# Kernel optimization log

Measured on AMD Instinct MI355X. Metric: run time of the kernel, lower is better.

Reference implementation:

```python
import jax, jax.numpy as jnp
import numpy as np

# Poincare ball manifold with curvature c = 1.0 (as in HGCN / HADA)
C = 1.0
SQC = 1.0  # sqrt(c)
MIN_NORM = 1e-15
PROJ_EPS = 4e-3  # float32 boundary eps used by HGCN PoincareBall.proj


def _norm(x):
    return jnp.clip(jnp.linalg.norm(x, axis=-1, keepdims=True), MIN_NORM)


def artanh(x):
    return jnp.arctanh(jnp.clip(x, -1.0 + 1e-7, 1.0 - 1e-7))


def proj(x):
    n = _norm(x)
    maxnorm = (1.0 - PROJ_EPS) / SQC
    return jnp.where(n > maxnorm, x / n * maxnorm, x)


def proj_tan0(u):
    return u  # identity on the Poincare ball


def expmap0(u):
    n = _norm(u)
    return jnp.tanh(SQC * n) * u / (SQC * n)


def logmap0(p):
    n = _norm(p)
    return artanh(SQC * n) * p / (SQC * n)


def mobius_add(x, y):
    x2 = jnp.sum(x * x, axis=-1, keepdims=True)
    y2 = jnp.sum(y * y, axis=-1, keepdims=True)
    xy = jnp.sum(x * y, axis=-1, keepdims=True)
    num = (1.0 + 2.0 * C * xy + C * y2) * x + (1.0 - C * x2) * y
    den = 1.0 + 2.0 * C * xy + C * C * x2 * y2
    return num / jnp.clip(den, MIN_NORM)


def mobius_matvec(M, x):
    xn = _norm(x)
    mx = x @ M.T
    mxn = _norm(mx)
    res = jnp.tanh(mxn / xn * artanh(SQC * xn)) * mx / (mxn * SQC)
    is_zero = jnp.all(mx == 0.0, axis=-1, keepdims=True)
    return jnp.where(is_zero, jnp.zeros_like(res), res)


def lambda_x(x):
    return 2.0 / jnp.clip(1.0 - C * jnp.sum(x * x, axis=-1, keepdims=True), MIN_NORM)


def expmap(x, u):
    n = _norm(u)
    second = jnp.tanh(SQC * lambda_x(x) * n / 2.0) * u / (SQC * n)
    return mobius_add(x, second)


def logmap(x, y):
    sub = mobius_add(-x, y)
    n = _norm(sub)
    return 2.0 / (SQC * lambda_x(x)) * artanh(SQC * n) * sub / n


def setup_inputs() -> dict:
    key = jax.random.key(0)
    k1, k2, k3, k4, k5 = jax.random.split(key, 5)
    n, d_in, d_out = 1024, 128, 128
    # node features on the manifold
    x = proj(expmap0(0.1 * jax.random.normal(k1, (n, d_in), dtype=jnp.float32)))
    adj = (jax.random.uniform(k2, (n, n)) < 0.02).astype(jnp.float32)
    weight = 0.1 * jax.random.normal(k3, (d_out, d_in), dtype=jnp.float32)
    bias = 0.01 * jax.random.normal(k4, (d_out,), dtype=jnp.float32)
    att_w = 0.1 * jax.random.normal(k5, (1, 2 * d_out), dtype=jnp.float32)
    att_b = jnp.zeros((1,), dtype=jnp.float32)
    return {"x": x, "adj": adj, "weight": weight, "bias": bias,
            "att_w": att_w, "att_b": att_b}


def reference(x, adj, weight, bias, att_w, att_b):
    d_out = weight.shape[0]
    # --- HypLinear (dropout=0 / eval mode) ---
    mv = proj(mobius_matvec(weight, x))
    hyp_bias = proj(expmap0(proj_tan0(bias[None, :])))
    h = proj(mobius_add(mv, hyp_bias))  # [n, d]
    # --- HypAgg: use_att=True, local_agg=True ---
    x_tangent = logmap0(h)  # [n, d]
    # pairwise logmap: x_local[i, j] = logmap(h[i], h[j])  -> [n, n, d]
    x_local = jax.vmap(lambda xi: logmap(xi, h))(h)
    # DenseAtt: sigmoid(W [x_i ; x_j] + b), decomposed into left/right parts
    wl, wr = att_w[0, :d_out], att_w[0, d_out:]
    logits = (x_tangent @ wl)[:, None] + (x_tangent @ wr)[None, :] + att_b[0]
    adj_att = adj * jax.nn.sigmoid(logits)  # [n, n]
    support_t = jnp.einsum('ij,ijd->id', adj_att, x_local)  # [n, d]
    h_agg = proj(expmap(h, support_t))
    # --- HypAct (as written in source: activation result is discarded,
    # proj_tan0 is applied to the layer input; proj_tan0 = identity) ---
    out = proj(expmap0(proj_tan0(h_agg)))
    return out
```

## Files before the change

kernel.cpp:

```cpp
#include <hip/hip_runtime.h>
#include <math.h>

#define N 1024
#define D 128
#define CAP 96
#define MAXNORM 0.996f
#define MINN 1e-15f

__device__ __forceinline__ float wave_sum(float v) {
#pragma unroll
    for (int o = 32; o > 0; o >>= 1) v += __shfl_xor(v, o, 64);
    return v;
}

__device__ __forceinline__ void wave_sum2(float& a, float& b) {
#pragma unroll
    for (int o = 32; o > 0; o >>= 1) {
        a += __shfl_xor(a, o, 64);
        b += __shfl_xor(b, o, 64);
    }
}

__device__ __forceinline__ float group16_sum(float v) {
#pragma unroll
    for (int o = 8; o > 0; o >>= 1) v += __shfl_xor(v, o, 64);
    return v;
}

__device__ __forceinline__ float artanh_fast(float x) {
    x = fminf(fmaxf(x, -1.0f + 1e-7f), 1.0f - 1e-7f);
    return 0.5f * __logf(__fdividef(1.0f + x, 1.0f - x));
}

__global__ __launch_bounds__(256) void k_rows(
    const float* __restrict__ x, const float* __restrict__ Wm,
    const float* __restrict__ bias, const float* __restrict__ attw,
    const float* __restrict__ adj, float* __restrict__ h,
    float* __restrict__ h2a, float* __restrict__ sLa, float* __restrict__ sRa,
    int* __restrict__ cnt_g, int* __restrict__ lst_g,
    float* __restrict__ vals_g) {
    __shared__ float smv[D];
    __shared__ int wcnt[4];
    const int t = threadIdx.x, w = t >> 6, l = t & 63;
    const int g = l >> 4, m = l & 15;
    const int i = blockIdx.x;
    const unsigned long long lt_mask = (1ull << l) - 1ull;

    float4 av = *(const float4*)(adj + (size_t)i * N + (w << 8) + 4 * l);

    float4 xa = *(const float4*)(x + (size_t)i * D + 4 * m);
    float4 xb = *(const float4*)(x + (size_t)i * D + 64 + 4 * m);

    float xn2 = group16_sum(xa.x * xa.x + xa.y * xa.y + xa.z * xa.z +
                            xa.w * xa.w + xb.x * xb.x + xb.y * xb.y +
                            xb.z * xb.z + xb.w * xb.w);

#pragma unroll
    for (int p = 0; p < 8; ++p) {
        const int o = (w << 5) + (p << 2) + g;
        float4 wa = *(const float4*)(Wm + (size_t)o * D + 4 * m);
        float4 wb = *(const float4*)(Wm + (size_t)o * D + 64 + 4 * m);
        float s = xa.x * wa.x + xa.y * wa.y + xa.z * wa.z + xa.w * wa.w +
                  xb.x * wb.x + xb.y * wb.y + xb.z * wb.z + xb.w * wb.w;
        s = group16_sum(s);
        if (m == 0) smv[o] = s;
    }

    float ae[4] = {av.x, av.y, av.z, av.w};
    unsigned long long msk[4];
    int cnt = 0;
#pragma unroll
    for (int e = 0; e < 4; ++e) {
        msk[e] = __ballot(ae[e] != 0.0f);
        cnt += __popcll(msk[e]);
    }
    if (l == 0) wcnt[w] = cnt;
    __syncthreads();

    int base = 0;
#pragma unroll
    for (int ww = 0; ww < 4; ++ww)
        if (ww < w) base += wcnt[ww];
    const int tot = wcnt[0] + wcnt[1] + wcnt[2] + wcnt[3];
    {
        int off = base;
#pragma unroll
        for (int e = 0; e < 4; ++e) {
            if (ae[e] != 0.0f) {
                int pos = off + __popcll(msk[e] & lt_mask);
                if (pos < CAP) {
                    lst_g[i * CAP + pos] = (w << 8) + 4 * l + e;
                    vals_g[i * CAP + pos] = ae[e];
                }
            }
            off += __popcll(msk[e]);
        }
    }
    if (t == 0) cnt_g[i] = (tot < CAP) ? tot : CAP;

    if (w != 0) return;

    float2 bv = *(const float2*)(bias + 2 * l);
    float bn2 = wave_sum(bv.x * bv.x + bv.y * bv.y);
    float bn = fmaxf(sqrtf(bn2), MINN);
    float tb = tanhf(bn);
    float bs = tb / bn;
    float2 hbv = make_float2(bs * bv.x, bs * bv.y);
    float vn = tb;
    if (vn > MAXNORM) {
        float sc0 = MAXNORM / vn;
        hbv.x *= sc0; hbv.y *= sc0;
        vn = MAXNORM;
    }
    float y2 = vn * vn;

    float2 mv = *(const float2*)(&smv[2 * l]);
    float mxn2 = wave_sum(mv.x * mv.x + mv.y * mv.y);
    float mxn = fmaxf(sqrtf(mxn2), MINN);
    float xn = fmaxf(sqrtf(xn2), MINN);
    float rn = tanhf(mxn / xn * artanh_fast(xn));
    float sc = rn / mxn;
    float r0 = sc * mv.x, r1 = sc * mv.y;
    float sr = (rn > MAXNORM) ? (MAXNORM / rn) : 1.f;
    r0 *= sr; r1 *= sr;
    float rn_c = rn * sr;
    float x2 = rn_c * rn_c;

    float xy = wave_sum(r0 * hbv.x + r1 * hbv.y);
    float den = fmaxf(1.f + 2.f * xy + x2 * y2, MINN);
    float ca = (1.f + 2.f * xy + y2) / den;
    float cb = (1.f - x2) / den;
    float hp0 = ca * r0 + cb * hbv.x;
    float hp1 = ca * r1 + cb * hbv.y;
    float hn2 = wave_sum(hp0 * hp0 + hp1 * hp1);
    float hn = fmaxf(sqrtf(hn2), MINN);
    float sh = (hn > MAXNORM) ? (MAXNORM / hn) : 1.f;
    hp0 *= sh; hp1 *= sh;
    float h2 = hn2 * sh * sh;

    float hnn = fmaxf(sqrtf(h2), MINN);
    float fac = artanh_fast(hnn) / hnn;
    float dwl = wave_sum(hp0 * attw[2 * l] + hp1 * attw[2 * l + 1]);
    float dwr = wave_sum(hp0 * attw[D + 2 * l] + hp1 * attw[D + 2 * l + 1]);

    *(float2*)(h + (size_t)i * D + 2 * l) = make_float2(hp0, hp1);
    if (l == 0) {
        h2a[i] = h2;
        sLa[i] = fac * dwl;
        sRa[i] = fac * dwr;
    }
}

__global__ __launch_bounds__(256) void k_agg(
    const float* __restrict__ h, const float* __restrict__ h2a,
    const float* __restrict__ sLa, const float* __restrict__ sRa,
    const int* __restrict__ cnt_g, const int* __restrict__ lst_g,
    const float* __restrict__ vals_g, const float* __restrict__ attb_p,
    float* __restrict__ out) {
    __shared__ float accS[16][132];
    __shared__ float sAs[16];

    const int t = threadIdx.x, w = t >> 6, l = t & 63;
    const int gid = t >> 4, m = t & 15;
    const int i = blockIdx.x;

    const int tot = cnt_g[i];
    const float h2_i = h2a[i];
    const float sL_i = sLa[i];
    const float attb = attb_p[0];
    const float B = 1.f - h2_i;
    const float cA = fmaxf(B, MINN);

    float4 hi0 = *(const float4*)(h + (size_t)i * D + 8 * m);
    float4 hi1 = *(const float4*)(h + (size_t)i * D + 8 * m + 4);

    float4 a0 = make_float4(0.f, 0.f, 0.f, 0.f);
    float4 a1 = make_float4(0.f, 0.f, 0.f, 0.f);
    float sAcc = 0.f;

    for (int n = gid; n < tot; n += 16) {
        const int j = lst_g[i * CAP + n];
        const float aval = vals_g[i * CAP + n];
        float4 hj0 = *(const float4*)(h + (size_t)j * D + 8 * m);
        float4 hj1 = *(const float4*)(h + (size_t)j * D + 8 * m + 4);
        float d = hi0.x * hj0.x + hi0.y * hj0.y + hi0.z * hj0.z +
                  hi0.w * hj0.w + hi1.x * hj1.x + hi1.y * hj1.y +
                  hi1.z * hj1.z + hi1.w * hj1.w;
        float dot = group16_sum(d);
        float h2_j = h2a[j];
        float sR_j = sRa[j];
        float den = fmaxf(1.f - 2.f * dot + h2_i * h2_j, MINN);
        float p = __fdividef(-(1.f - 2.f * dot + h2_j), den);
        float q = __fdividef(B, den);
        float n2 = p * p * h2_i + 2.f * p * q * dot + q * q * h2_j;
        float nrm = fmaxf(sqrtf(fmaxf(n2, 0.f)), MINN);
        float coefc = cA * __fdividef(artanh_fast(nrm), nrm);
        float sig = __fdividef(1.f, 1.f + __expf(-(sL_i + sR_j + attb)));
        float wgt = aval * sig;
        sAcc += wgt * coefc * p;
        float wb = wgt * coefc * q;
        a0.x += wb * hj0.x; a0.y += wb * hj0.y;
        a0.z += wb * hj0.z; a0.w += wb * hj0.w;
        a1.x += wb * hj1.x; a1.y += wb * hj1.y;
        a1.z += wb * hj1.z; a1.w += wb * hj1.w;
    }

    *(float4*)(&accS[gid][8 * m]) = a0;
    *(float4*)(&accS[gid][8 * m + 4]) = a1;
    if (m == 0) sAs[gid] = sAcc;
    __syncthreads();

    if (w != 0) return;

    float b0 = 0.f, b1 = 0.f, sA = 0.f;
#pragma unroll
    for (int g2 = 0; g2 < 16; ++g2) {
        b0 += accS[g2][2 * l];
        b1 += accS[g2][2 * l + 1];
        sA += sAs[g2];
    }

    float2 hi = *(const float2*)(h + (size_t)i * D + 2 * l);
    float u0 = sA * hi.x + b0, u1 = sA * hi.y + b1;

    float u2 = u0 * u0 + u1 * u1;
    float hiu = hi.x * u0 + hi.y * u1;
    wave_sum2(u2, hiu);
    float un = fmaxf(sqrtf(u2), MINN);
    float lam = 2.f / cA;
    float th = tanhf(0.5f * lam * un);
    float r = th / un;
    float s0 = r * u0, s1 = r * u1;
    float y2 = th * th;
    float xy = r * hiu;
    float den2 = fmaxf(1.f + 2.f * xy + h2_i * y2, MINN);
    float c1 = (1.f + 2.f * xy + y2) / den2;
    float c2 = (1.f - h2_i) / den2;
    float hp0 = c1 * hi.x + c2 * s0;
    float hp1 = c1 * hi.y + c2 * s1;
    float hn2 = wave_sum(hp0 * hp0 + hp1 * hp1);
    float hn = fmaxf(sqrtf(hn2), MINN);
    float scl = (hn > MAXNORM) ? (MAXNORM / hn) : 1.f;
    hp0 *= scl; hp1 *= scl;
    float n3 = fminf(fmaxf(hn, MINN), MAXNORM);
    float fac = tanhf(n3) / n3;
    float o0 = fac * hp0, o1 = fac * hp1;
    float onrm = tanhf(n3);
    if (onrm > MAXNORM) {
        float ss = MAXNORM / onrm;
        o0 *= ss; o1 *= ss;
    }
    *(float2*)(out + (size_t)i * D + 2 * l) = make_float2(o0, o1);
}

extern "C" void kernel_launch(void* const* d_in, const int* in_sizes, int n_in,
                              void* d_out, int out_size, void* d_ws, size_t ws_size,
                              hipStream_t stream) {
    const float* x = (const float*)d_in[0];
    const float* adj = (const float*)d_in[1];
    const float* Wm = (const float*)d_in[2];
    const float* bias = (const float*)d_in[3];
    const float* attw = (const float*)d_in[4];
    const float* attb = (const float*)d_in[5];
    float* out = (float*)d_out;

    float* ws = (float*)d_ws;
    float* h = ws;
    float* h2a = h + (size_t)N * D;
    float* sL = h2a + N;
    float* sR = sL + N;
    float* vals_g = sR + N;
    int* cnt_g = (int*)(vals_g + (size_t)N * CAP);
    int* lst_g = cnt_g + N;

    hipLaunchKernelGGL(k_rows, dim3(N), dim3(256), 0, stream, x, Wm, bias, attw,
                       adj, h, h2a, sL, sR, cnt_g, lst_g, vals_g);
    hipLaunchKernelGGL(k_agg, dim3(N), dim3(256), 0, stream, h, h2a, sL, sR,
                       cnt_g, lst_g, vals_g, attb, out);
}
```

Before: 17.75 us.

## Pack edge data, precompute sigmoid exponentials, widen per-lane slices in aggregation

Edge index and value are packed into one int2, and h2 is stored together with exp(-sR) so the aggregation loop does fewer separate loads. The sigmoid now factors into precomputed per-row exponentials exp(-(sL+attb)) times exp(-sR), which removes an exp per edge. In k_agg each neighbour is handled by 8 lanes holding 16 floats each instead of 16 lanes holding 8, giving 32 neighbour groups per block and shorter shuffle reductions. k_rows also merges its wave reductions into fewer shuffle passes. The wider slices use more registers, and the final reduction now sums over 32 groups instead of 16.

```diff
diff --git a/kernel.cpp b/kernel.cpp
--- a/kernel.cpp
+++ b/kernel.cpp
@@ -21,9 +21,24 @@
     }
 }
 
+__device__ __forceinline__ void wave_sum3(float& a, float& b, float& c) {
+#pragma unroll
+    for (int o = 32; o > 0; o >>= 1) {
+        a += __shfl_xor(a, o, 64);
+        b += __shfl_xor(b, o, 64);
+        c += __shfl_xor(c, o, 64);
+    }
+}
+
 __device__ __forceinline__ float group16_sum(float v) {
 #pragma unroll
     for (int o = 8; o > 0; o >>= 1) v += __shfl_xor(v, o, 64);
+    return v;
+}
+
+__device__ __forceinline__ float group8_sum(float v) {
+#pragma unroll
+    for (int o = 4; o > 0; o >>= 1) v += __shfl_xor(v, o, 64);
     return v;
 }
 
@@ -35,10 +50,9 @@
 __global__ __launch_bounds__(256) void k_rows(
     const float* __restrict__ x, const float* __restrict__ Wm,
     const float* __restrict__ bias, const float* __restrict__ attw,
-    const float* __restrict__ adj, float* __restrict__ h,
-    float* __restrict__ h2a, float* __restrict__ sLa, float* __restrict__ sRa,
-    int* __restrict__ cnt_g, int* __restrict__ lst_g,
-    float* __restrict__ vals_g) {
+    const float* __restrict__ attb_p, const float* __restrict__ adj,
+    float* __restrict__ h, float2* __restrict__ hsc, float* __restrict__ ELa,
+    int* __restrict__ cnt_g, int2* __restrict__ edge_g) {
     __shared__ float smv[D];
     __shared__ int wcnt[4];
     const int t = threadIdx.x, w = t >> 6, l = t & 63;
@@ -88,10 +102,9 @@
         for (int e = 0; e < 4; ++e) {
             if (ae[e] != 0.0f) {
                 int pos = off + __popcll(msk[e] & lt_mask);
-                if (pos < CAP) {
-                    lst_g[i * CAP + pos] = (w << 8) + 4 * l + e;
-                    vals_g[i * CAP + pos] = ae[e];
-                }
+                if (pos < CAP)
+                    edge_g[i * CAP + pos] =
+                        make_int2((w << 8) + 4 * l + e, __float_as_int(ae[e]));
             }
             off += __popcll(msk[e]);
         }
@@ -100,8 +113,14 @@
 
     if (w != 0) return;
 
+    const float attb = attb_p[0];
     float2 bv = *(const float2*)(bias + 2 * l);
-    float bn2 = wave_sum(bv.x * bv.x + bv.y * bv.y);
+    float2 mv = *(const float2*)(&smv[2 * l]);
+
+    float mxn2 = mv.x * mv.x + mv.y * mv.y;
+    float bn2 = bv.x * bv.x + bv.y * bv.y;
+    wave_sum2(mxn2, bn2);
+
     float bn = fmaxf(sqrtf(bn2), MINN);
     float tb = tanhf(bn);
     float bs = tb / bn;
@@ -114,8 +133,6 @@
     }
     float y2 = vn * vn;
 
-    float2 mv = *(const float2*)(&smv[2 * l]);
-    float mxn2 = wave_sum(mv.x * mv.x + mv.y * mv.y);
     float mxn = fmaxf(sqrtf(mxn2), MINN);
     float xn = fmaxf(sqrtf(xn2), MINN);
     float rn = tanhf(mxn / xn * artanh_fast(xn));
@@ -132,81 +149,101 @@
     float cb = (1.f - x2) / den;
     float hp0 = ca * r0 + cb * hbv.x;
     float hp1 = ca * r1 + cb * hbv.y;
-    float hn2 = wave_sum(hp0 * hp0 + hp1 * hp1);
-    float hn = fmaxf(sqrtf(hn2), MINN);
+
+    float t0 = hp0 * hp0 + hp1 * hp1;
+    float t1 = hp0 * attw[2 * l] + hp1 * attw[2 * l + 1];
+    float t2 = hp0 * attw[D + 2 * l] + hp1 * attw[D + 2 * l + 1];
+    wave_sum3(t0, t1, t2);
+
+    float hn = fmaxf(sqrtf(t0), MINN);
     float sh = (hn > MAXNORM) ? (MAXNORM / hn) : 1.f;
     hp0 *= sh; hp1 *= sh;
-    float h2 = hn2 * sh * sh;
-
+    float h2 = t0 * sh * sh;
     float hnn = fmaxf(sqrtf(h2), MINN);
     float fac = artanh_fast(hnn) / hnn;
-    float dwl = wave_sum(hp0 * attw[2 * l] + hp1 * attw[2 * l + 1]);
-    float dwr = wave_sum(hp0 * attw[D + 2 * l] + hp1 * attw[D + 2 * l + 1]);
+    float sLv = fac * (t1 * sh);
+    float sRv = fac * (t2 * sh);
 
     *(float2*)(h + (size_t)i * D + 2 * l) = make_float2(hp0, hp1);
     if (l == 0) {
-        h2a[i] = h2;
-        sLa[i] = fac * dwl;
-        sRa[i] = fac * dwr;
+        hsc[i] = make_float2(h2, __expf(-sRv));
+        ELa[i] = __expf(-(sLv + attb));
     }
 }
 
 __global__ __launch_bounds__(256) void k_agg(
-    const float* __restrict__ h, const float* __restrict__ h2a,
-    const float* __restrict__ sLa, const float* __restrict__ sRa,
-    const int* __restrict__ cnt_g, const int* __restrict__ lst_g,
-    const float* __restrict__ vals_g, const float* __restrict__ attb_p,
-    float* __restrict__ out) {
-    __shared__ float accS[16][132];
-    __shared__ float sAs[16];
+    const float* __restrict__ h, const float2* __restrict__ hsc,
+    const float* __restrict__ ELa, const int* __restrict__ cnt_g,
+    const int2* __restrict__ edge_g, float* __restrict__ out) {
+    __shared__ __align__(16) float accS[32][132];
+    __shared__ float sAs[32];
 
     const int t = threadIdx.x, w = t >> 6, l = t & 63;
-    const int gid = t >> 4, m = t & 15;
+    const int gid = t >> 3, m = t & 7;
     const int i = blockIdx.x;
 
     const int tot = cnt_g[i];
-    const float h2_i = h2a[i];
-    const float sL_i = sLa[i];
-    const float attb = attb_p[0];
+    const float2 qi = hsc[i];
+    const float h2_i = qi.x;
+    const float EL_i = ELa[i];
     const float B = 1.f - h2_i;
     const float cA = fmaxf(B, MINN);
 
-    float4 hi0 = *(const float4*)(h + (size_t)i * D + 8 * m);
-    float4 hi1 = *(const float4*)(h + (size_t)i * D + 8 * m + 4);
+    const float* hrow = h + (size_t)i * D + 16 * m;
+    float4 hi0 = *(const float4*)(hrow);
+    float4 hi1 = *(const float4*)(hrow + 4);
+    float4 hi2 = *(const float4*)(hrow + 8);
+    float4 hi3 = *(const float4*)(hrow + 12);
 
     float4 a0 = make_float4(0.f, 0.f, 0.f, 0.f);
     float4 a1 = make_float4(0.f, 0.f, 0.f, 0.f);
+    float4 a2 = make_float4(0.f, 0.f, 0.f, 0.f);
+    float4 a3 = make_float4(0.f, 0.f, 0.f, 0.f);
     float sAcc = 0.f;
 
-    for (int n = gid; n < tot; n += 16) {
-        const int j = lst_g[i * CAP + n];
-        const float aval = vals_g[i * CAP + n];
-        float4 hj0 = *(const float4*)(h + (size_t)j * D + 8 * m);
-        float4 hj1 = *(const float4*)(h + (size_t)j * D + 8 * m + 4);
+    for (int n = gid; n < tot; n += 32) {
+        int2 e = edge_g[i * CAP + n];
+        const int j = e.x;
+        const float aval = __int_as_float(e.y);
+        const float* hj = h + (size_t)j * D + 16 * m;
+        float4 hj0 = *(const float4*)(hj);
+        float4 hj1 = *(const float4*)(hj + 4);
+        float4 hj2 = *(const float4*)(hj + 8);
+        float4 hj3 = *(const float4*)(hj + 12);
+        float2 qj = hsc[j];
+
         float d = hi0.x * hj0.x + hi0.y * hj0.y + hi0.z * hj0.z +
                   hi0.w * hj0.w + hi1.x * hj1.x + hi1.y * hj1.y +
-                  hi1.z * hj1.z + hi1.w * hj1.w;
-        float dot = group16_sum(d);
-        float h2_j = h2a[j];
-        float sR_j = sRa[j];
+                  hi1.z * hj1.z + hi1.w * hj1.w + hi2.x * hj2.x +
+                  hi2.y * hj2.y + hi2.z * hj2.z + hi2.w * hj2.w +
+                  hi3.x * hj3.x + hi3.y * hj3.y + hi3.z * hj3.z +
+                  hi3.w * hj3.w;
+        float dot = group8_sum(d);
+        float h2_j = qj.x, ER_j = qj.y;
         float den = fmaxf(1.f - 2.f * dot + h2_i * h2_j, MINN);
         float p = __fdividef(-(1.f - 2.f * dot + h2_j), den);
-        float q = __fdividef(B, den);
-        float n2 = p * p * h2_i + 2.f * p * q * dot + q * q * h2_j;
+        float qq = __fdividef(B, den);
+        float n2 = p * p * h2_i + 2.f * p * qq * dot + qq * qq * h2_j;
         float nrm = fmaxf(sqrtf(fmaxf(n2, 0.f)), MINN);
         float coefc = cA * __fdividef(artanh_fast(nrm), nrm);
-        float sig = __fdividef(1.f, 1.f + __expf(-(sL_i + sR_j + attb)));
+        float sig = __fdividef(1.f, 1.f + EL_i * ER_j);
         float wgt = aval * sig;
         sAcc += wgt * coefc * p;
-        float wb = wgt * coefc * q;
+        float wb = wgt * coefc * qq;
         a0.x += wb * hj0.x; a0.y += wb * hj0.y;
         a0.z += wb * hj0.z; a0.w += wb * hj0.w;
         a1.x += wb * hj1.x; a1.y += wb * hj1.y;
         a1.z += wb * hj1.z; a1.w += wb * hj1.w;
-    }
-
-    *(float4*)(&accS[gid][8 * m]) = a0;
-    *(float4*)(&accS[gid][8 * m + 4]) = a1;
+        a2.x += wb * hj2.x; a2.y += wb * hj2.y;
+        a2.z += wb * hj2.z; a2.w += wb * hj2.w;
+        a3.x += wb * hj3.x; a3.y += wb * hj3.y;
+        a3.z += wb * hj3.z; a3.w += wb * hj3.w;
+    }
+
+    *(float4*)(&accS[gid][16 * m]) = a0;
+    *(float4*)(&accS[gid][16 * m + 4]) = a1;
+    *(float4*)(&accS[gid][16 * m + 8]) = a2;
+    *(float4*)(&accS[gid][16 * m + 12]) = a3;
     if (m == 0) sAs[gid] = sAcc;
     __syncthreads();
 
@@ -214,7 +251,7 @@
 
     float b0 = 0.f, b1 = 0.f, sA = 0.f;
 #pragma unroll
-    for (int g2 = 0; g2 < 16; ++g2) {
+    for (int g2 = 0; g2 < 32; ++g2) {
         b0 += accS[g2][2 * l];
         b1 += accS[g2][2 * l + 1];
         sA += sAs[g2];
@@ -266,15 +303,13 @@
 
     float* ws = (float*)d_ws;
     float* h = ws;
-    float* h2a = h + (size_t)N * D;
-    float* sL = h2a + N;
-    float* sR = sL + N;
-    float* vals_g = sR + N;
-    int* cnt_g = (int*)(vals_g + (size_t)N * CAP);
-    int* lst_g = cnt_g + N;
-
-    hipLaunchKernelGGL(k_rows, dim3(N), dim3(256), 0, stream, x, Wm, bias, attw,
-                       adj, h, h2a, sL, sR, cnt_g, lst_g, vals_g);
-    hipLaunchKernelGGL(k_agg, dim3(N), dim3(256), 0, stream, h, h2a, sL, sR,
-                       cnt_g, lst_g, vals_g, attb, out);
-}
+    float2* hsc = (float2*)(h + (size_t)N * D);
+    float* ELa = (float*)(hsc + N);
+    int* cnt_g = (int*)(ELa + N);
+    int2* edge_g = (int2*)(cnt_g + N);
+
+    hipLaunchKernelGGL(k_rows, dim3(N), dim3(256), 0, stream, x, Wm, bias,
+                       attw, attb, adj, h, hsc, ELa, cnt_g, edge_g);
+    hipLaunchKernelGGL(k_agg, dim3(N), dim3(256), 0, stream, h, hsc, ELa,
+                       cnt_g, edge_g, out);
+}
```

After: 17.43 us. No clear change (-1.8%).
